# Optimization experiments

Measured on AMD Instinct MI355X. Metric: run time of the kernel, lower is better.

Reference implementation:

```python
import math
import jax, jax.numpy as jnp
import numpy as np

EPS = 1e-5  # torch LayerNorm default
K_MA = 25   # moving-average kernel


def _layernorm(x, g, b):
    mu = x.mean(-1, keepdims=True)
    var = ((x - mu) ** 2).mean(-1, keepdims=True)
    return (x - mu) * jax.lax.rsqrt(var + EPS) * g + b


def _moving_avg(x, k=K_MA):
    # x: [B, L, C]; edge-replicate pad (k-1)//2 on both sides, avg window k, stride 1
    pad = (k - 1) // 2
    front = jnp.repeat(x[:, :1], pad, axis=1)
    back = jnp.repeat(x[:, -1:], pad, axis=1)
    xp = jnp.concatenate([front, x, back], axis=1)          # [B, L+2*pad, C]
    cs = jnp.cumsum(xp, axis=1)
    cs = jnp.concatenate([jnp.zeros_like(cs[:, :1]), cs], axis=1)
    return (cs[:, k:] - cs[:, :-k]) / k                     # [B, L, C]


def _autocorrelation(q, k, v, factor=1):
    # q,k,v: [B, L, H, D] -> FFT cross-correlation along time, top-k lag aggregation (inference path)
    B, L, H, D = q.shape
    qp = q.transpose(0, 2, 3, 1)                            # [B,H,D,L]
    kp = k.transpose(0, 2, 3, 1)
    vp = v.transpose(0, 2, 3, 1)
    qf = jnp.fft.rfft(qp, axis=-1)
    kf = jnp.fft.rfft(kp, axis=-1)
    corr = jnp.fft.irfft(qf * jnp.conj(kf), n=L, axis=-1)   # [B,H,D,L]

    top_k = int(factor * math.log(L))
    mean_corr = corr.mean(axis=(1, 2))                      # [B,L]
    weights, delay = jax.lax.top_k(mean_corr, top_k)        # [B,k]
    alpha = jax.nn.softmax(weights, axis=-1)                # [B,k]

    base = jnp.arange(L)
    agg = jnp.zeros_like(vp)
    for i in range(top_k):  # small static loop (top_k = 7)
        idx = (base[None, :] + delay[:, i:i + 1]) % L       # circular gather == roll by -delay
        gathered = jnp.take_along_axis(vp, idx[:, None, None, :], axis=-1)
        agg = agg + gathered * alpha[:, i][:, None, None, None]
    return agg.transpose(0, 3, 1, 2)                        # [B,L,H,D]


def _forward(x, Wq, Wk, Wv, Wo, bo, ln_g, ln_b, W1, W2, num_heads=16, factor=1):
    B, L, C = x.shape
    H = num_heads
    D = C // H
    xn = _layernorm(x, ln_g, ln_b)
    q = jnp.einsum('blc,oc->blo', xn, Wq).reshape(B, L, H, D)
    k = jnp.einsum('blc,oc->blo', xn, Wk).reshape(B, L, H, D)
    v = jnp.einsum('blc,oc->blo', xn, Wv).reshape(B, L, H, D)
    agg = _autocorrelation(q, k, v, factor=factor).reshape(B, L, C)
    attn_out = jnp.einsum('blc,oc->blo', agg, Wo) + bo
    x = x + attn_out
    x = x - _moving_avg(x)                                  # decomp1 seasonal part
    # FFN: 1x1 convs == linear layers, exact GELU (torch default)
    y = jax.nn.gelu(jnp.einsum('blc,hc->blh', x, W1), approximate=False)
    y = jnp.einsum('blh,ch->blc', y, W2)
    x = x + y
    x = x - _moving_avg(x)                                  # decomp2 seasonal part
    return x


def setup_inputs() -> dict:
    key = jax.random.key(0)
    ks = jax.random.split(key, 8)
    B, L, C = 8, 2048, 1024
    Hd = 4 * C
    s = 0.02
    return {
        'x': jax.random.normal(ks[0], (B, L, C), dtype=jnp.float32),
        'Wq': jax.random.normal(ks[1], (C, C), dtype=jnp.float32) * s,
        'Wk': jax.random.normal(ks[2], (C, C), dtype=jnp.float32) * s,
        'Wv': jax.random.normal(ks[3], (C, C), dtype=jnp.float32) * s,
        'Wo': jax.random.normal(ks[4], (C, C), dtype=jnp.float32) * s,
        'bo': jnp.zeros((C,), dtype=jnp.float32),
        'ln_g': jnp.ones((C,), dtype=jnp.float32),
        'ln_b': jnp.zeros((C,), dtype=jnp.float32),
        'W1': jax.random.normal(ks[5], (Hd, C), dtype=jnp.float32) * s,
        'W2': jax.random.normal(ks[6], (C, Hd), dtype=jnp.float32) * s,
    }


def reference(x, Wq, Wk, Wv, Wo, bo, ln_g, ln_b, W1, W2):
    return _forward(x, Wq, Wk, Wv, Wo, bo, ln_g, ln_b, W1, W2)
```

## Files before the change

kernel.cpp:

```cpp
#include <hip/hip_runtime.h>
#include <cstdint>
#include <cstddef>


typedef _Float16 half8 __attribute__((ext_vector_type(8)));
typedef _Float16 half4 __attribute__((ext_vector_type(4)));
typedef float floatx4 __attribute__((ext_vector_type(4)));

#define PI_F 3.14159265358979323846f
#define ZP32(i) ((i) + ((i) >> 5))

__device__ __forceinline__ void load_lds16(const void* g, void* l) {
  __builtin_amdgcn_global_load_lds((__attribute__((address_space(1))) void*)g,
                                   (__attribute__((address_space(3))) void*)l,
                                   16, 0, 0);
}


__global__ __launch_bounds__(256) void cvt_f16_kernel(const float* __restrict__ src,
                                                      _Float16* __restrict__ dst, int n4) {
  int i = blockIdx.x * 256 + threadIdx.x;
  if (i >= n4) return;
  float4 v = ((const float4*)src)[i];
  half4 h = {(_Float16)v.x, (_Float16)v.y, (_Float16)v.z, (_Float16)v.w};
  ((half4*)dst)[i] = h;
}

__global__ __launch_bounds__(256) void transpose_f16_kernel(const float* __restrict__ src,
                                                            _Float16* __restrict__ dst, int n) {
  __shared__ float tile[64][65];
  int j0 = blockIdx.y * 64, c0 = blockIdx.x * 64;
  int tr = threadIdx.x >> 4;
  int tc = threadIdx.x & 15;
#pragma unroll
  for (int rr = 0; rr < 64; rr += 16) {
    float4 v = *(const float4*)(src + (size_t)(j0 + tr + rr) * n + c0 + tc * 4);
    tile[tr + rr][tc * 4 + 0] = v.x;
    tile[tr + rr][tc * 4 + 1] = v.y;
    tile[tr + rr][tc * 4 + 2] = v.z;
    tile[tr + rr][tc * 4 + 3] = v.w;
  }
  __syncthreads();
#pragma unroll
  for (int rr = 0; rr < 64; rr += 16) {
    int c = tr + rr;
    half4 h = {(_Float16)tile[tc * 4 + 0][c], (_Float16)tile[tc * 4 + 1][c],
               (_Float16)tile[tc * 4 + 2][c], (_Float16)tile[tc * 4 + 3][c]};
    *(half4*)(dst + (size_t)(c0 + c) * n + j0 + tc * 4) = h;
  }
}

__global__ __launch_bounds__(256) void ln_kernel(const float* __restrict__ x,
                                                 const float* __restrict__ g,
                                                 const float* __restrict__ b,
                                                 _Float16* __restrict__ xn, int C) {
  int row = blockIdx.x;
  int t = threadIdx.x;
  const float4* xr = (const float4*)(x + (size_t)row * C);
  float4 v = xr[t];
  float s = v.x + v.y + v.z + v.w;
  float s2 = v.x * v.x + v.y * v.y + v.z * v.z + v.w * v.w;
  for (int o = 32; o > 0; o >>= 1) {
    s += __shfl_down(s, o, 64);
    s2 += __shfl_down(s2, o, 64);
  }
  __shared__ float red[8];
  int wave = t >> 6, lane = t & 63;
  if (lane == 0) { red[wave] = s; red[4 + wave] = s2; }
  __syncthreads();
  __shared__ float stats[2];
  if (t == 0) {
    float ts = red[0] + red[1] + red[2] + red[3];
    float ts2 = red[4] + red[5] + red[6] + red[7];
    float mu = ts / (float)C;
    float var = ts2 / (float)C - mu * mu;
    stats[0] = mu;
    stats[1] = 1.0f / sqrtf(var + 1e-5f);
  }
  __syncthreads();
  float mu = stats[0], rs = stats[1];
  float4 gv = ((const float4*)g)[t];
  float4 bv = ((const float4*)b)[t];
  half4 h = {(_Float16)((v.x - mu) * rs * gv.x + bv.x),
             (_Float16)((v.y - mu) * rs * gv.y + bv.y),
             (_Float16)((v.z - mu) * rs * gv.z + bv.z),
             (_Float16)((v.w - mu) * rs * gv.w + bv.w)};
  ((half4*)(xn + (size_t)row * C))[t] = h;
}

template <int EPI>
__global__ __launch_bounds__(512, 2) void gemm256_kernel(
    const _Float16* __restrict__ A, const _Float16* __restrict__ Bw,
    int M, int N, int K, int lda, int ldb,
    float* __restrict__ outf, _Float16* __restrict__ outh,
    const float* __restrict__ bias, const float* __restrict__ res) {
  __shared__ _Float16 lds[2][2][256 * 64];

  int tid = threadIdx.x;
  int lane = tid & 63;
  int wave = tid >> 6;
  int wm = wave >> 2;
  int wn = wave & 3;
  int ln15 = lane & 15, q4 = lane >> 4;
  int l3 = lane >> 3, l7 = lane & 7;

  int nwg = gridDim.x, orig = blockIdx.x;
  int wg = ((nwg & 7) == 0) ? ((orig & 7) * (nwg >> 3) + (orig >> 3)) : orig;
  int nbn = N >> 8;
  size_t m0 = (size_t)(wg / nbn) << 8;
  size_t n0 = (size_t)(wg % nbn) << 8;

  int sg0 = (q4 ^ l7) << 3;
  int sg1 = ((q4 + 4) ^ l7) << 3;

  floatx4 acc[8][4] = {};

  const _Float16* srcA = A + (m0 + 8 * wave + l3) * (size_t)lda + (size_t)((l7 ^ l3) * 8);
  const _Float16* srcB = Bw + (n0 + 8 * wave + l3) * (size_t)ldb + (size_t)((l7 ^ l3) * 8);
  char* ldsA0 = (char*)&lds[0][0][0] + wave * 1024;
  char* ldsB0 = (char*)&lds[0][1][0] + wave * 1024;

  load_lds16(srcB, ldsB0);
  load_lds16(srcB + (size_t)64 * ldb, ldsB0 + 1 * 8192);
  load_lds16(srcB + (size_t)128 * ldb, ldsB0 + 2 * 8192);
  load_lds16(srcB + (size_t)192 * ldb, ldsB0 + 3 * 8192);
  load_lds16(srcA, ldsA0);
  load_lds16(srcA + (size_t)128 * lda, ldsA0 + 2 * 8192);
  load_lds16(srcA + (size_t)64 * lda, ldsA0 + 1 * 8192);
  load_lds16(srcA + (size_t)192 * lda, ldsA0 + 3 * 8192);
  asm volatile("s_waitcnt vmcnt(2)" ::: "memory");
  __builtin_amdgcn_s_barrier();
  __builtin_amdgcn_sched_barrier(0);

  int nk = K >> 6;
  half8 bf[4][2], aA[2][2];

#define RD_B() _Pragma("unroll") for (int ni = 0; ni < 4; ++ni) {      \
    const _Float16* p_ = cB + ((wn * 64 + ni * 16 + ln15) << 6);       \
    bf[ni][0] = *(const half8*)(p_ + sg0);                             \
    bf[ni][1] = *(const half8*)(p_ + sg1); }
#define RD_A(mi) { const _Float16* p_ = cA + ((wm * 128 + (mi) * 16 + ln15) << 6); \
    aA[(mi) & 1][0] = *(const half8*)(p_ + sg0);                                   \
    aA[(mi) & 1][1] = *(const half8*)(p_ + sg1); }
#define MM(mi) _Pragma("unroll") for (int ni = 0; ni < 4; ++ni) {      \
    acc[mi][ni] = __builtin_amdgcn_mfma_f32_16x16x32_f16(aA[(mi) & 1][0], bf[ni][0], acc[mi][ni], 0, 0, 0); \
    acc[mi][ni] = __builtin_amdgcn_mfma_f32_16x16x32_f16(aA[(mi) & 1][1], bf[ni][1], acc[mi][ni], 0, 0, 0); }

#define PH_MID()                                            \
    __builtin_amdgcn_s_barrier();                           \
    asm volatile("s_waitcnt lgkmcnt(0)" ::: "memory");      \
    __builtin_amdgcn_sched_barrier(0);                      \
    __builtin_amdgcn_s_setprio(1);
#define PH_END()                                            \
    __builtin_amdgcn_s_setprio(0);                          \
    __builtin_amdgcn_s_barrier();                           \
    __builtin_amdgcn_sched_barrier(0);

  for (int t = 0; t < nk; ++t) {
    int cur = t & 1;
    const _Float16* cA = &lds[cur][0][0];
    const _Float16* cB = &lds[cur][1][0];
    const _Float16* As = srcA + (size_t)(t + 1) * 64;
    const _Float16* Bs = srcB + (size_t)(t + 1) * 64;
    char* stA = ldsA0 + (cur ^ 1) * 65536;
    char* stB = ldsB0 + (cur ^ 1) * 65536;
    bool pf = (t + 1 < nk);

    RD_B();
    RD_A(0); RD_A(1);
    if (pf) {
      load_lds16(Bs, stB);
      load_lds16(Bs + (size_t)64 * ldb, stB + 1 * 8192);
      load_lds16(Bs + (size_t)128 * ldb, stB + 2 * 8192);
    }
    PH_MID();
    MM(0); MM(1);
    PH_END();
    RD_A(2); RD_A(3);
    if (pf) {
      load_lds16(Bs + (size_t)192 * ldb, stB + 3 * 8192);
      load_lds16(As, stA);
      load_lds16(As + (size_t)128 * lda, stA + 2 * 8192);
    }
    PH_MID();
    MM(2); MM(3);
    __builtin_amdgcn_s_setprio(0);
    if (pf) {
      asm volatile("s_waitcnt vmcnt(6)" ::: "memory");
    } else {
      asm volatile("s_waitcnt vmcnt(0)" ::: "memory");
    }
    __builtin_amdgcn_s_barrier();
    __builtin_amdgcn_sched_barrier(0);
    RD_A(4); RD_A(5);
    if (pf) {
      load_lds16(As + (size_t)64 * lda, stA + 1 * 8192);
    }
    PH_MID();
    MM(4); MM(5);
    PH_END();
    RD_A(6); RD_A(7);
    if (pf) {
      load_lds16(As + (size_t)192 * lda, stA + 3 * 8192);
    }
    PH_MID();
    MM(6); MM(7);
    __builtin_amdgcn_s_setprio(0);
    asm volatile("s_waitcnt vmcnt(2)" ::: "memory");
    __builtin_amdgcn_s_barrier();
    __builtin_amdgcn_sched_barrier(0);
  }
#undef RD_B
#undef RD_A
#undef MM
#undef PH_MID
#undef PH_END

#pragma unroll
  for (int mi = 0; mi < 8; ++mi) {
#pragma unroll
    for (int ni = 0; ni < 4; ++ni) {
      floatx4 a4 = acc[mi][ni];
      size_t rowb = m0 + wm * 128 + mi * 16 + q4 * 4;
      size_t col = n0 + wn * 64 + ni * 16 + ln15;
      if (EPI == 5) {
        size_t b = rowb >> 11, l0 = rowb & 2047;
        half4 h = {(_Float16)a4[0], (_Float16)a4[1], (_Float16)a4[2], (_Float16)a4[3]};
        *(half4*)(outh + (((size_t)b * N + col) << 11) + l0) = h;
      } else {
#pragma unroll
        for (int r = 0; r < 4; ++r) {
          size_t idx = (rowb + r) * (size_t)N + col;
          float v = a4[r];
          if (EPI == 1) {
            outf[idx] = v + bias[col] + res[idx];
          } else if (EPI == 2) {
            float ge = 0.5f * v * (1.0f + erff(v * 0.70710678118654752f));
            outh[idx] = (_Float16)ge;
          } else if (EPI == 3) {
            outf[idx] = v + res[idx];
          } else {
            outh[idx] = (_Float16)v;
          }
        }
      }
    }
  }
}


#define CBFLY(ch, ia, ib, wr, wi) {                      \
    float ax_ = z[ch][ia].x, ay_ = z[ch][ia].y;          \
    float bx_ = z[ch][ib].x, by_ = z[ch][ib].y;          \
    float dx_ = ax_ - bx_, dy_ = ay_ - by_;              \
    z[ch][ia].x = ax_ + bx_; z[ch][ia].y = ay_ + by_;    \
    z[ch][ib].x = dx_ * (wr) - dy_ * (wi);               \
    z[ch][ib].y = dx_ * (wi) + dy_ * (wr); }
#define BFLY2(ia, ib, m) { float2 w_ = twl[ZP32(m)];     \
    CBFLY(0, ia, ib, w_.x, w_.y) CBFLY(1, ia, ib, w_.x, w_.y) }

__global__ __launch_bounds__(256) void corr_fft_kernel(const _Float16* __restrict__ F,
                                                       float* __restrict__ S) {
  __shared__ float2 Zs[2][2112];
  __shared__ float2 twl[1056];
  int tid = threadIdx.x;
  int b = blockIdx.x >> 9;
  int c0 = (blockIdx.x & 511) << 1;
  const _Float16* qb = F + ((size_t)(b * 2048 + c0) << 11);
  const _Float16* kb = F + ((size_t)(b * 2048 + 1024 + c0) << 11);

  float2 z[2][8];
#pragma unroll
  for (int j = 0; j < 8; ++j) {
    int p = tid + 256 * j;
    z[0][j] = make_float2((float)qb[p], (float)kb[p]);
    z[1][j] = make_float2((float)qb[2048 + p], (float)kb[2048 + p]);
  }
  for (int m = tid; m < 1024; m += 256) {
    float sn, cs;
    __sincosf(-PI_F * (float)m / 1024.0f, &sn, &cs);
    twl[ZP32(m)] = make_float2(cs, sn);
  }
  __syncthreads();

  BFLY2(0, 4, tid)
  BFLY2(1, 5, tid + 256)
  BFLY2(2, 6, tid + 512)
  BFLY2(3, 7, tid + 768)
  { float2 wA = twl[ZP32(tid << 1)], wB = twl[ZP32((tid + 256) << 1)];
    CBFLY(0, 0, 2, wA.x, wA.y) CBFLY(1, 0, 2, wA.x, wA.y)
    CBFLY(0, 1, 3, wB.x, wB.y) CBFLY(1, 1, 3, wB.x, wB.y)
    CBFLY(0, 4, 6, wA.x, wA.y) CBFLY(1, 4, 6, wA.x, wA.y)
    CBFLY(0, 5, 7, wB.x, wB.y) CBFLY(1, 5, 7, wB.x, wB.y) }
  { float2 wA = twl[ZP32(tid << 2)];
    CBFLY(0, 0, 1, wA.x, wA.y) CBFLY(1, 0, 1, wA.x, wA.y)
    CBFLY(0, 2, 3, wA.x, wA.y) CBFLY(1, 2, 3, wA.x, wA.y)
    CBFLY(0, 4, 5, wA.x, wA.y) CBFLY(1, 4, 5, wA.x, wA.y)
    CBFLY(0, 6, 7, wA.x, wA.y) CBFLY(1, 6, 7, wA.x, wA.y) }

#pragma unroll
  for (int j = 0; j < 8; ++j) {
    int p = tid + 256 * j;
    Zs[0][ZP32(p)] = z[0][j];
    Zs[1][ZP32(p)] = z[1][j];
  }
  __syncthreads();
  int t5 = tid & 31, hi1 = (tid >> 5) << 8;
#pragma unroll
  for (int j = 0; j < 8; ++j) {
    int p = hi1 + t5 + 32 * j;
    z[0][j] = Zs[0][ZP32(p)];
    z[1][j] = Zs[1][ZP32(p)];
  }

  BFLY2(0, 4, t5 << 3)
  BFLY2(1, 5, (t5 + 32) << 3)
  BFLY2(2, 6, (t5 + 64) << 3)
  BFLY2(3, 7, (t5 + 96) << 3)
  { float2 wA = twl[ZP32(t5 << 4)], wB = twl[ZP32((t5 + 32) << 4)];
    CBFLY(0, 0, 2, wA.x, wA.y) CBFLY(1, 0, 2, wA.x, wA.y)
    CBFLY(0, 1, 3, wB.x, wB.y) CBFLY(1, 1, 3, wB.x, wB.y)
    CBFLY(0, 4, 6, wA.x, wA.y) CBFLY(1, 4, 6, wA.x, wA.y)
    CBFLY(0, 5, 7, wB.x, wB.y) CBFLY(1, 5, 7, wB.x, wB.y) }
  { float2 wA = twl[ZP32(t5 << 5)];
    CBFLY(0, 0, 1, wA.x, wA.y) CBFLY(1, 0, 1, wA.x, wA.y)
    CBFLY(0, 2, 3, wA.x, wA.y) CBFLY(1, 2, 3, wA.x, wA.y)
    CBFLY(0, 4, 5, wA.x, wA.y) CBFLY(1, 4, 5, wA.x, wA.y)
    CBFLY(0, 6, 7, wA.x, wA.y) CBFLY(1, 6, 7, wA.x, wA.y) }

#pragma unroll
  for (int j = 0; j < 8; ++j) {
    int p = hi1 + t5 + 32 * j;
    Zs[0][ZP32(p)] = z[0][j];
    Zs[1][ZP32(p)] = z[1][j];
  }
  __syncthreads();
  int t3 = tid & 3, hi2 = (tid >> 2) << 5;
#pragma unroll
  for (int j = 0; j < 8; ++j) {
    int p = hi2 + t3 + 4 * j;
    z[0][j] = Zs[0][ZP32(p)];
    z[1][j] = Zs[1][ZP32(p)];
  }

  BFLY2(0, 4, t3 << 6)
  BFLY2(1, 5, (t3 + 4) << 6)
  BFLY2(2, 6, (t3 + 8) << 6)
  BFLY2(3, 7, (t3 + 12) << 6)
  { float2 wA = twl[ZP32(t3 << 7)], wB = twl[ZP32((t3 + 4) << 7)];
    CBFLY(0, 0, 2, wA.x, wA.y) CBFLY(1, 0, 2, wA.x, wA.y)
    CBFLY(0, 1, 3, wB.x, wB.y) CBFLY(1, 1, 3, wB.x, wB.y)
    CBFLY(0, 4, 6, wA.x, wA.y) CBFLY(1, 4, 6, wA.x, wA.y)
    CBFLY(0, 5, 7, wB.x, wB.y) CBFLY(1, 5, 7, wB.x, wB.y) }
  { float2 wA = twl[ZP32(t3 << 8)];
    CBFLY(0, 0, 1, wA.x, wA.y) CBFLY(1, 0, 1, wA.x, wA.y)
    CBFLY(0, 2, 3, wA.x, wA.y) CBFLY(1, 2, 3, wA.x, wA.y)
    CBFLY(0, 4, 5, wA.x, wA.y) CBFLY(1, 4, 5, wA.x, wA.y)
    CBFLY(0, 6, 7, wA.x, wA.y) CBFLY(1, 6, 7, wA.x, wA.y) }

#pragma unroll
  for (int j = 0; j < 8; ++j) {
    int p = hi2 + t3 + 4 * j;
    Zs[0][ZP32(p)] = z[0][j];
    Zs[1][ZP32(p)] = z[1][j];
  }
  __syncthreads();
#pragma unroll
  for (int j = 0; j < 8; ++j) {
    int p = (tid << 3) + j;
    z[0][j] = Zs[0][ZP32(p)];
    z[1][j] = Zs[1][ZP32(p)];
  }

  CBFLY(0, 0, 2, 1.0f, 0.0f) CBFLY(1, 0, 2, 1.0f, 0.0f)
  CBFLY(0, 1, 3, 0.0f, -1.0f) CBFLY(1, 1, 3, 0.0f, -1.0f)
  CBFLY(0, 4, 6, 1.0f, 0.0f) CBFLY(1, 4, 6, 1.0f, 0.0f)
  CBFLY(0, 5, 7, 0.0f, -1.0f) CBFLY(1, 5, 7, 0.0f, -1.0f)
  CBFLY(0, 0, 1, 1.0f, 0.0f) CBFLY(1, 0, 1, 1.0f, 0.0f)
  CBFLY(0, 2, 3, 1.0f, 0.0f) CBFLY(1, 2, 3, 1.0f, 0.0f)
  CBFLY(0, 4, 5, 1.0f, 0.0f) CBFLY(1, 4, 5, 1.0f, 0.0f)
  CBFLY(0, 6, 7, 1.0f, 0.0f) CBFLY(1, 6, 7, 1.0f, 0.0f)

#pragma unroll
  for (int j = 0; j < 8; ++j) {
    int p = (tid << 3) + j;
    Zs[0][ZP32(p)] = z[0][j];
    Zs[1][ZP32(p)] = z[1][j];
  }
  __syncthreads();
  float* Sb = S + (size_t)blockIdx.x * 2050;
  for (int f = tid; f <= 1024; f += 256) {
    int rf = __brev((unsigned)f) >> 21;
    int rmf = __brev((unsigned)((2048 - f) & 2047)) >> 21;
    float pr = 0.f, pim = 0.f;
#pragma unroll
    for (int ch = 0; ch < 2; ++ch) {
      float2 zf = Zs[ch][ZP32(rf)], zm = Zs[ch][ZP32(rmf)];
      float Qr = 0.5f * (zf.x + zm.x), Qi = 0.5f * (zf.y - zm.y);
      float Kr = 0.5f * (zf.y + zm.y), Ki = -0.5f * (zf.x - zm.x);
      pr += Qr * Kr + Qi * Ki;
      pim += Qi * Kr - Qr * Ki;
    }
    Sb[2 * f] = pr;
    Sb[2 * f + 1] = pim;
  }
}

__global__ __launch_bounds__(256) void spec_reduce_kernel(const float* __restrict__ Sbig,
                                                          float* __restrict__ S8) {
  int f = blockIdx.x * 256 + threadIdx.x;
  int sc = blockIdx.y;
  int b = blockIdx.z;
  if (f >= 2050) return;
  const float* src = Sbig + ((size_t)b * 512 + (size_t)sc * 64) * 2050 + f;
  float s = 0.f;
  for (int i = 0; i < 64; ++i) s += src[(size_t)i * 2050];
  S8[((size_t)b * 8 + sc) * 2050 + f] = s;
}

__global__ __launch_bounds__(256) void corr_topk_kernel(const float* __restrict__ S,
                                                        int* __restrict__ delays,
                                                        float* __restrict__ alphas,
                                                        int C, int L) {
  __shared__ float2 W[2048];
  __shared__ float mc[2048];
  __shared__ float rv[4];
  __shared__ int ri[4];
  __shared__ float swv[7];
  __shared__ int sdi[7];
  int b = blockIdx.x, tid = threadIdx.x;
  const float* Sb = S + (size_t)b * 8 * 2050;
  for (int f = tid; f < 2048; f += 256) {
    int ff = f <= 1024 ? f : 2048 - f;
    float re = 0.f, im = 0.f;
    for (int s = 0; s < 8; ++s) {
      re += Sb[s * 2050 + 2 * ff];
      im += Sb[s * 2050 + 2 * ff + 1];
    }
    W[f] = make_float2(re, f <= 1024 ? -im : im);
  }
  __syncthreads();
  for (int sh = 10; sh >= 0; --sh) {
    int s = 1 << sh;
    for (int j = tid; j < 1024; j += 256) {
      int t = j & (s - 1);
      int i0 = ((j >> sh) << (sh + 1)) | t;
      int i1 = i0 + s;
      float2 a = W[i0], bb = W[i1];
      float ang = -PI_F * (float)t / (float)s;
      float sn, cs;
      __sincosf(ang, &sn, &cs);
      float2 d = make_float2(a.x - bb.x, a.y - bb.y);
      W[i0] = make_float2(a.x + bb.x, a.y + bb.y);
      W[i1] = make_float2(d.x * cs - d.y * sn, d.x * sn + d.y * cs);
    }
    __syncthreads();
  }
  float inv = 1.0f / ((float)C * (float)L);
  for (int t = tid; t < 2048; t += 256) mc[t] = W[__brev((unsigned)t) >> 21].x * inv;
  __syncthreads();
  int wv = tid >> 6, lane = tid & 63;
  for (int it = 0; it < 7; ++it) {
    float bvv = -1e30f;
    int bi = 0;
    for (int e = tid * 8; e < tid * 8 + 8; ++e) {
      float v = mc[e];
      if (v > bvv) { bvv = v; bi = e; }
    }
    for (int o = 32; o > 0; o >>= 1) {
      float ov = __shfl_down(bvv, o, 64);
      int oi = __shfl_down(bi, o, 64);
      if (ov > bvv || (ov == bvv && oi < bi)) { bvv = ov; bi = oi; }
    }
    if (lane == 0) { rv[wv] = bvv; ri[wv] = bi; }
    __syncthreads();
    if (tid == 0) {
      float fv = rv[0];
      int fi = ri[0];
      for (int w2 = 1; w2 < 4; ++w2)
        if (rv[w2] > fv || (rv[w2] == fv && ri[w2] < fi)) { fv = rv[w2]; fi = ri[w2]; }
      swv[it] = fv;
      sdi[it] = fi;
      mc[fi] = -1e30f;
    }
    __syncthreads();
  }
  if (tid == 0) {
    float mx = swv[0];
    for (int i = 1; i < 7; ++i) mx = fmaxf(mx, swv[i]);
    float e[7], s = 0.f;
    for (int i = 0; i < 7; ++i) { e[i] = expf(swv[i] - mx); s += e[i]; }
    for (int i = 0; i < 7; ++i) {
      alphas[b * 7 + i] = e[i] / s;
      delays[b * 7 + i] = sdi[i];
    }
  }
}

__global__ __launch_bounds__(256) void agg_kernel(const _Float16* __restrict__ v,
                                                  const int* __restrict__ delays,
                                                  const float* __restrict__ alphas,
                                                  _Float16* __restrict__ agg,
                                                  int L, int C) {
  int bt = blockIdx.x;
  int b = bt >> 11, t = bt & 2047;
  int tid = threadIdx.x;
  const _Float16* vb = v + (size_t)b * L * C;
  float ax = 0.f, ay = 0.f, az = 0.f, aw = 0.f;
#pragma unroll
  for (int i = 0; i < 7; ++i) {
    int d = delays[b * 7 + i];
    float a = alphas[b * 7 + i];
    int src = t + d;
    if (src >= L) src -= L;
    half4 x = ((const half4*)(vb + (size_t)src * C))[tid];
    ax += a * (float)x.x; ay += a * (float)x.y;
    az += a * (float)x.z; aw += a * (float)x.w;
  }
  half4 h = {(_Float16)ax, (_Float16)ay, (_Float16)az, (_Float16)aw};
  ((half4*)(agg + (size_t)bt * C))[tid] = h;
}

template <int WRITE_H>
__global__ __launch_bounds__(256) void decomp_kernel(const float* __restrict__ xin,
                                                     float* __restrict__ xout,
                                                     _Float16* __restrict__ xh,
                                                     int L, int C) {
  int c = blockIdx.x * 256 + threadIdx.x;
  int t0 = blockIdx.y * 128;
  int b = blockIdx.z;
  const float* xb = xin + (size_t)b * L * C + c;
  float sum = 0.f;
  for (int j = t0 - 12; j <= t0 + 12; ++j) {
    int jc = j < 0 ? 0 : (j > L - 1 ? L - 1 : j);
    sum += xb[(size_t)jc * C];
  }
  for (int t = t0; t < t0 + 128; ++t) {
    float xv = xb[(size_t)t * C];
    float o = xv - sum * (1.0f / 25.0f);
    size_t oidx = ((size_t)b * L + t) * C + c;
    xout[oidx] = o;
    if (WRITE_H) xh[oidx] = (_Float16)o;
    int nj = t + 13; if (nj > L - 1) nj = L - 1;
    int oj = t - 12; if (oj < 0) oj = 0;
    sum += xb[(size_t)nj * C] - xb[(size_t)oj * C];
  }
}

extern "C" void kernel_launch(void* const* d_in, const int* in_sizes, int n_in,
                              void* d_out, int out_size, void* d_ws, size_t ws_size,
                              hipStream_t stream) {
  const float* x = (const float*)d_in[0];
  const float* Wq = (const float*)d_in[1];
  const float* Wk = (const float*)d_in[2];
  const float* Wv = (const float*)d_in[3];
  const float* Wo = (const float*)d_in[4];
  const float* bo = (const float*)d_in[5];
  const float* lng = (const float*)d_in[6];
  const float* lnb = (const float*)d_in[7];
  const float* W1 = (const float*)d_in[8];
  const float* W2 = (const float*)d_in[9];
  float* out = (float*)d_out;

  const int B = 8, L = 2048, C = 1024, HD = 4096;
  const int M = B * L;

  char* ws = (char*)d_ws;
  size_t off = 0;
  auto alloc = [&](size_t bytes) -> void* {
    void* p = ws + off;
    off = (off + bytes + 255) & ~(size_t)255;
    return p;
  };
  _Float16* wqkh = (_Float16*)alloc((size_t)2 * C * C * 2);
  _Float16* wvoh = (_Float16*)alloc((size_t)C * C * 2);
  _Float16* w1h = (_Float16*)alloc((size_t)HD * C * 2);
  _Float16* w2h = (_Float16*)alloc((size_t)C * HD * 2);
  float* S8 = (float*)alloc((size_t)B * 8 * 2050 * 4);
  int* dl = (int*)alloc(B * 7 * 4);
  float* al = (float*)alloc(B * 7 * 4);
  _Float16* xn = (_Float16*)alloc((size_t)M * C * 2);
  _Float16* qkh = (_Float16*)alloc((size_t)M * 2 * C * 2);
  _Float16* vh = (_Float16*)alloc((size_t)4096 * 2050 * 4);
  (void)ws_size; (void)in_sizes; (void)n_in; (void)out_size;

  _Float16* wvT = vh;
  _Float16* woh = vh + (size_t)C * C;
  float* Sbig = (float*)vh;
  _Float16* aggh = vh;
  float* x1 = (float*)qkh;
  _Float16* x2h = xn;
  float* x2 = out;
  float* x3 = (float*)qkh;
  _Float16* hidc = vh;

  cvt_f16_kernel<<<(C * C / 4 + 255) / 256, 256, 0, stream>>>(Wq, wqkh, C * C / 4);
  cvt_f16_kernel<<<(C * C / 4 + 255) / 256, 256, 0, stream>>>(Wk, wqkh + (size_t)C * C, C * C / 4);
  cvt_f16_kernel<<<(C * C / 4 + 255) / 256, 256, 0, stream>>>(Wo, woh, C * C / 4);
  transpose_f16_kernel<<<dim3(16, 16), 256, 0, stream>>>(Wv, wvT, C);
  cvt_f16_kernel<<<(HD * C / 4 + 255) / 256, 256, 0, stream>>>(W1, w1h, HD * C / 4);
  cvt_f16_kernel<<<(HD * C / 4 + 255) / 256, 256, 0, stream>>>(W2, w2h, HD * C / 4);
  gemm256_kernel<4><<<16, 512, 0, stream>>>(woh, wvT, C, C, C, C, C,
                                            nullptr, wvoh, nullptr, nullptr);
  ln_kernel<<<M, 256, 0, stream>>>(x, lng, lnb, xn, C);
  gemm256_kernel<5><<<(M / 256) * (2 * C / 256), 512, 0, stream>>>(
      xn, wqkh, M, 2 * C, C, C, C, nullptr, qkh, nullptr, nullptr);
  corr_fft_kernel<<<B * (C / 2), 256, 0, stream>>>(qkh, Sbig);
  spec_reduce_kernel<<<dim3(9, 8, 8), 256, 0, stream>>>(Sbig, S8);
  corr_topk_kernel<<<B, 256, 0, stream>>>(S8, dl, al, C, L);
  agg_kernel<<<B * L, 256, 0, stream>>>(xn, dl, al, aggh, L, C);
  gemm256_kernel<1><<<(M / 256) * (C / 256), 512, 0, stream>>>(
      aggh, wvoh, M, C, C, C, C, x1, nullptr, bo, x);
  decomp_kernel<1><<<dim3(C / 256, L / 128, B), 256, 0, stream>>>(x1, x2, x2h, L, C);
  for (int ci = 0; ci < 4; ++ci) {
    gemm256_kernel<2><<<(M / 256) * (1024 / 256), 512, 0, stream>>>(
        x2h, w1h + (size_t)ci * 1024 * C, M, 1024, C, C, C,
        nullptr, hidc, nullptr, nullptr);
    gemm256_kernel<3><<<(M / 256) * (C / 256), 512, 0, stream>>>(
        hidc, w2h + (size_t)ci * 1024, M, C, 1024, 1024, HD,
        x3, nullptr, nullptr, ci == 0 ? x2 : x3);
  }
  decomp_kernel<0><<<dim3(C / 256, L / 128, B), 256, 0, stream>>>(x3, out, nullptr, L, C);
}
```

Before: 930.6 us.

## Split FFN into two 2048-wide chunks with fp16 residual accumulator

The FFN hidden dimension is now processed in two chunks of 2048 instead of four chunks of 1024, which halves the number of GEMM launches and partial-sum passes. The running FFN output (residual plus partial W2 products) is kept in fp16 instead of fp32, using new epilogues that add the residual or the previous partial and write half precision. A new decomposition kernel reads that fp16 buffer. This cuts memory traffic for the accumulator, but rounds the residual stream to fp16 between chunks, which may cost accuracy.

```diff
diff --git a/kernel.cpp b/kernel.cpp
--- a/kernel.cpp
+++ b/kernel.cpp
@@ -237,8 +237,11 @@
           } else if (EPI == 2) {
             float ge = 0.5f * v * (1.0f + erff(v * 0.70710678118654752f));
             outh[idx] = (_Float16)ge;
-          } else if (EPI == 3) {
-            outf[idx] = v + res[idx];
+          } else if (EPI == 6) {
+            outh[idx] = (_Float16)(v + res[idx]);
+          } else if (EPI == 7) {
+            float prev = (float)outh[idx];
+            outh[idx] = (_Float16)(v + prev);
           } else {
             outh[idx] = (_Float16)v;
           }
@@ -547,6 +550,28 @@
   }
 }
 
+__global__ __launch_bounds__(256) void decomp_h_kernel(const _Float16* __restrict__ xin,
+                                                       float* __restrict__ xout,
+                                                       int L, int C) {
+  int c = blockIdx.x * 256 + threadIdx.x;
+  int t0 = blockIdx.y * 128;
+  int b = blockIdx.z;
+  const _Float16* xb = xin + (size_t)b * L * C + c;
+  float sum = 0.f;
+  for (int j = t0 - 12; j <= t0 + 12; ++j) {
+    int jc = j < 0 ? 0 : (j > L - 1 ? L - 1 : j);
+    sum += (float)xb[(size_t)jc * C];
+  }
+  for (int t = t0; t < t0 + 128; ++t) {
+    float xv = (float)xb[(size_t)t * C];
+    float o = xv - sum * (1.0f / 25.0f);
+    xout[((size_t)b * L + t) * C + c] = o;
+    int nj = t + 13; if (nj > L - 1) nj = L - 1;
+    int oj = t - 12; if (oj < 0) oj = 0;
+    sum += (float)xb[(size_t)nj * C] - (float)xb[(size_t)oj * C];
+  }
+}
+
 extern "C" void kernel_launch(void* const* d_in, const int* in_sizes, int n_in,
                               void* d_out, int out_size, void* d_ws, size_t ws_size,
                               hipStream_t stream) {
@@ -591,8 +616,8 @@
   float* x1 = (float*)qkh;
   _Float16* x2h = xn;
   float* x2 = out;
-  float* x3 = (float*)qkh;
-  _Float16* hidc = vh;
+  _Float16* hid2 = qkh;
+  _Float16* x3h = vh;
 
   cvt_f16_kernel<<<(C * C / 4 + 255) / 256, 256, 0, stream>>>(Wq, wqkh, C * C / 4);
   cvt_f16_kernel<<<(C * C / 4 + 255) / 256, 256, 0, stream>>>(Wk, wqkh + (size_t)C * C, C * C / 4);
@@ -612,13 +637,17 @@
   gemm256_kernel<1><<<(M / 256) * (C / 256), 512, 0, stream>>>(
       aggh, wvoh, M, C, C, C, C, x1, nullptr, bo, x);
   decomp_kernel<1><<<dim3(C / 256, L / 128, B), 256, 0, stream>>>(x1, x2, x2h, L, C);
-  for (int ci = 0; ci < 4; ++ci) {
-    gemm256_kernel<2><<<(M / 256) * (1024 / 256), 512, 0, stream>>>(
-        x2h, w1h + (size_t)ci * 1024 * C, M, 1024, C, C, C,
-        nullptr, hidc, nullptr, nullptr);
-    gemm256_kernel<3><<<(M / 256) * (C / 256), 512, 0, stream>>>(
-        hidc, w2h + (size_t)ci * 1024, M, C, 1024, 1024, HD,
-        x3, nullptr, nullptr, ci == 0 ? x2 : x3);
-  }
-  decomp_kernel<0><<<dim3(C / 256, L / 128, B), 256, 0, stream>>>(x3, out, nullptr, L, C);
-}
+  for (int ci = 0; ci < 2; ++ci) {
+    gemm256_kernel<2><<<(M / 256) * (2048 / 256), 512, 0, stream>>>(
+        x2h, w1h + (size_t)ci * 2048 * C, M, 2048, C, C, C,
+        nullptr, hid2, nullptr, nullptr);
+    if (ci == 0) {
+      gemm256_kernel<6><<<(M / 256) * (C / 256), 512, 0, stream>>>(
+          hid2, w2h, M, C, 2048, 2048, HD, nullptr, x3h, nullptr, x2);
+    } else {
+      gemm256_kernel<7><<<(M / 256) * (C / 256), 512, 0, stream>>>(
+          hid2, w2h + 2048, M, C, 2048, 2048, HD, nullptr, x3h, nullptr, nullptr);
+    }
+  }
+  decomp_h_kernel<<<dim3(C / 256, L / 128, B), 256, 0, stream>>>(x3h, out, L, C);
+}
```

After: 886.7 us. -4.7%, faster.
